# Kernel tuning notes

Hardware: AMD Instinct MI355X
Metric: run time of the kernel (lower is better)

## Reference

```python
import jax, jax.numpy as jnp
import numpy as np

ALPHA = 1.0

def setup_inputs() -> dict:
    key = jax.random.key(0)
    k1, k2 = jax.random.split(key)
    x = jax.random.normal(k1, (65536, 256), dtype=jnp.float32)
    clusters = jax.random.normal(k2, (512, 256), dtype=jnp.float32)
    return {"x": x, "clusters": clusters}

def reference(x, clusters):
    # squared L2 distance without materializing [B, K, D] broadcasts:
    # d[b,k] = |x_b|^2 + |c_k|^2 - 2 x_b . c_k
    x_sq = jnp.sum(x * x, axis=1, keepdims=True)            # [B, 1]
    c_sq = jnp.sum(clusters * clusters, axis=1)[None, :]    # [1, K]
    cross = jnp.einsum('bd,kd->bk', x, clusters)            # [B, K]
    d = x_sq + c_sq - 2.0 * cross                           # [B, K]
    # Student-t kernel soft assignment
    q = (1.0 + d / ALPHA) ** (-(ALPHA + 1.0) / 2.0)
    q = q / jnp.sum(q, axis=1, keepdims=True)
    return q
```

## Files before the change

kernel.cpp:

```cpp
#include <hip/hip_runtime.h>
#include <hip/hip_bf16.h>

typedef __attribute__((ext_vector_type(8))) short bf16x8;
typedef __attribute__((ext_vector_type(4))) float f32x4;

#define K_DIM 256
#define N_DIM 512
#define BM 32
#define M_DIM 65536
#define TPB 8
#define GRID (M_DIM / BM / TPB)

__device__ __forceinline__ unsigned short f2bf(float f) {
    unsigned int u = __float_as_uint(f);
    unsigned int r = (u + 0x7fffu + ((u >> 16) & 1u)) >> 16;
    return (unsigned short)r;
}

__global__ __launch_bounds__(256) void prep_clusters(
        const float* __restrict__ clusters,
        unsigned short* __restrict__ cba,
        float* __restrict__ csq) {
    const int row = blockIdx.x;
    const int t = threadIdx.x;
    const float v = clusters[row * K_DIM + t];
    const int wc = row >> 6, n = (row >> 4) & 3, r = row & 15;
    const int ks = t >> 5, kh = (t >> 3) & 3, ko = t & 7;
    cba[(size_t)wc * 16384 + ks * 2048 + n * 512 + (kh * 16 + r) * 8 + ko] = f2bf(v);
    float s = v * v;
    #pragma unroll
    for (int m = 1; m < 64; m <<= 1) s += __shfl_xor(s, m);
    __shared__ float red[4];
    if ((t & 63) == 0) red[t >> 6] = s;
    __syncthreads();
    if (t == 0) csq[row] = red[0] + red[1] + red[2] + red[3];
}

__global__ __launch_bounds__(512, 2) void cluster_q(
        const float* __restrict__ x,
        const unsigned short* __restrict__ cba,
        const float* __restrict__ csq,
        float* __restrict__ out) {
    __shared__ __align__(16) unsigned short xa[BM * K_DIM];
    __shared__ float xsq[BM];
    __shared__ __align__(16) float csql[N_DIM];
    __shared__ float rsum[8][BM];

    const int t = threadIdx.x;
    const int lane = t & 63;
    const int wc = t >> 6;

    const unsigned short* gsrc = cba + (size_t)wc * 16384;
    bf16x8 breg[8][4];
    #pragma unroll
    for (int ks = 0; ks < 8; ++ks)
        #pragma unroll
        for (int n = 0; n < 4; ++n)
            breg[ks][n] = *reinterpret_cast<const bf16x8*>(
                              gsrc + ks * 2048 + n * 512 + lane * 8);

    csql[t] = csq[t];

    const size_t base = (size_t)blockIdx.x * (TPB * BM);

    float4 xr0, xr1, xr2, xr3;
    {
        const float4* xp = reinterpret_cast<const float4*>(x + (base + wc) * K_DIM);
        xr0 = xp[lane];
        xr1 = xp[512 + lane];
        xr2 = xp[1024 + lane];
        xr3 = xp[1536 + lane];
    }

    for (int it = 0; it < TPB; ++it) {
        const size_t rowbase = base + (size_t)it * BM;

        const float4 vv[4] = {xr0, xr1, xr2, xr3};
        #pragma unroll
        for (int p = 0; p < 4; ++p) {
            const int row = wc + p * 8;
            const float4 v = vv[p];
            float s = v.x * v.x + v.y * v.y + v.z * v.z + v.w * v.w;
            #pragma unroll
            for (int m = 1; m < 64; m <<= 1) s += __shfl_xor(s, m);
            if (lane == 0) xsq[row] = s;
            const ushort4 pk = make_ushort4(f2bf(v.x), f2bf(v.y), f2bf(v.z), f2bf(v.w));
            const int swz = (lane * 8) ^ ((row & 7) << 4);
            *reinterpret_cast<ushort4*>(reinterpret_cast<char*>(xa) + row * 512 + swz) = pk;
        }
        __syncthreads();

        if (it + 1 < TPB) {
            const float4* xp = reinterpret_cast<const float4*>(
                                   x + (rowbase + BM + wc) * K_DIM);
            xr0 = xp[lane];
            xr1 = xp[512 + lane];
            xr2 = xp[1024 + lane];
            xr3 = xp[1536 + lane];
        }
        __builtin_amdgcn_sched_barrier(0);

        f32x4 acc[2][4];
        #pragma unroll
        for (int m = 0; m < 2; ++m)
            #pragma unroll
            for (int n = 0; n < 4; ++n)
                acc[m][n] = (f32x4){0.f, 0.f, 0.f, 0.f};

        #pragma unroll
        for (int ks = 0; ks < 8; ++ks) {
            const int r0 = (lane & 15);
            const int r1 = 16 + (lane & 15);
            const int c0 = (ks * 64 + (lane >> 4) * 16) ^ ((r0 & 7) << 4);
            const int c1 = (ks * 64 + (lane >> 4) * 16) ^ ((r1 & 7) << 4);
            const bf16x8 xm0 = *reinterpret_cast<const bf16x8*>(
                                   reinterpret_cast<const char*>(xa) + r0 * 512 + c0);
            const bf16x8 xm1 = *reinterpret_cast<const bf16x8*>(
                                   reinterpret_cast<const char*>(xa) + r1 * 512 + c1);
            #pragma unroll
            for (int n = 0; n < 4; ++n) {
                acc[0][n] = __builtin_amdgcn_mfma_f32_16x16x32_bf16(breg[ks][n], xm0, acc[0][n], 0, 0, 0);
                acc[1][n] = __builtin_amdgcn_mfma_f32_16x16x32_bf16(breg[ks][n], xm1, acc[1][n], 0, 0, 0);
            }
        }

        const float4* csql4 = reinterpret_cast<const float4*>(csql);
        float part[2] = {0.f, 0.f};
        #pragma unroll
        for (int m = 0; m < 2; ++m) {
            const float xs1 = 1.f + xsq[m * 16 + (lane & 15)];
            #pragma unroll
            for (int n = 0; n < 4; ++n) {
                const float4 cs = csql4[wc * 16 + n * 4 + (lane >> 4)];
                f32x4 q;
                q[0] = __builtin_amdgcn_rcpf(fmaf(-2.f, acc[m][n][0], xs1 + cs.x));
                q[1] = __builtin_amdgcn_rcpf(fmaf(-2.f, acc[m][n][1], xs1 + cs.y));
                q[2] = __builtin_amdgcn_rcpf(fmaf(-2.f, acc[m][n][2], xs1 + cs.z));
                q[3] = __builtin_amdgcn_rcpf(fmaf(-2.f, acc[m][n][3], xs1 + cs.w));
                acc[m][n] = q;
                part[m] += (q[0] + q[1]) + (q[2] + q[3]);
            }
        }
        #pragma unroll
        for (int m = 0; m < 2; ++m) {
            float s = part[m];
            s += __shfl_xor(s, 16);
            s += __shfl_xor(s, 32);
            if (lane < 16) rsum[wc][m * 16 + lane] = s;
        }
        __syncthreads();

        #pragma unroll
        for (int m = 0; m < 2; ++m) {
            const int b = m * 16 + (lane & 15);
            const float inv = __builtin_amdgcn_rcpf(
                ((rsum[0][b] + rsum[1][b]) + (rsum[2][b] + rsum[3][b])) +
                ((rsum[4][b] + rsum[5][b]) + (rsum[6][b] + rsum[7][b])));
            float* orow = out + (rowbase + b) * N_DIM + wc * 64 + (lane >> 4) * 4;
            #pragma unroll
            for (int n = 0; n < 4; ++n) {
                const f32x4 v = acc[m][n];
                float4 st = make_float4(v[0] * inv, v[1] * inv, v[2] * inv, v[3] * inv);
                *reinterpret_cast<float4*>(orow + n * 16) = st;
            }
        }
    }
}

extern "C" void kernel_launch(void* const* d_in, const int* in_sizes, int n_in,
                              void* d_out, int out_size, void* d_ws, size_t ws_size,
                              hipStream_t stream) {
    const float* x        = (const float*)d_in[0];
    const float* clusters = (const float*)d_in[1];
    float* out = (float*)d_out;
    unsigned short* cba = (unsigned short*)d_ws;
    float* csq = (float*)((char*)d_ws + (size_t)N_DIM * K_DIM * 2);
    prep_clusters<<<N_DIM, K_DIM, 0, stream>>>(clusters, cba, csq);
    cluster_q<<<GRID, 512, 0, stream>>>(x, cba, csq, out);
}
```

Measured before the change: 53.38 us.

## Double-buffer x tile in LDS and drop one barrier per iteration

The LDS tile of x (plus its row norms and the row-sum scratch) becomes double-buffered. The next tile is converted to bf16 and stored into the alternate buffer while the current one feeds the MFMAs, and global prefetch now runs two tiles ahead. This removes the per-iteration barrier that separated the x staging from the matmul, leaving one lightweight LDS-only barrier per iteration. It doubles the x-tile LDS footprint and keeps more registers live, which could affect occupancy at two blocks per CU.

```diff
diff --git a/kernel.cpp b/kernel.cpp
--- a/kernel.cpp
+++ b/kernel.cpp
@@ -15,6 +15,11 @@
     unsigned int u = __float_as_uint(f);
     unsigned int r = (u + 0x7fffu + ((u >> 16) & 1u)) >> 16;
     return (unsigned short)r;
+}
+
+__device__ __forceinline__ void barrier_lds() {
+    asm volatile("s_waitcnt lgkmcnt(0)" ::: "memory");
+    __builtin_amdgcn_s_barrier();
 }
 
 __global__ __launch_bounds__(256) void prep_clusters(
@@ -41,10 +46,10 @@
         const unsigned short* __restrict__ cba,
         const float* __restrict__ csq,
         float* __restrict__ out) {
-    __shared__ __align__(16) unsigned short xa[BM * K_DIM];
-    __shared__ float xsq[BM];
+    __shared__ __align__(16) unsigned short xa[2][BM * K_DIM];
+    __shared__ float xsq[2][BM];
     __shared__ __align__(16) float csql[N_DIM];
-    __shared__ float rsum[8][BM];
+    __shared__ float rsum[2][8][BM];
 
     const int t = threadIdx.x;
     const int lane = t & 63;
@@ -66,15 +71,9 @@
     float4 xr0, xr1, xr2, xr3;
     {
         const float4* xp = reinterpret_cast<const float4*>(x + (base + wc) * K_DIM);
-        xr0 = xp[lane];
-        xr1 = xp[512 + lane];
-        xr2 = xp[1024 + lane];
-        xr3 = xp[1536 + lane];
-    }
-
-    for (int it = 0; it < TPB; ++it) {
-        const size_t rowbase = base + (size_t)it * BM;
-
+        xr0 = xp[lane]; xr1 = xp[512 + lane]; xr2 = xp[1024 + lane]; xr3 = xp[1536 + lane];
+    }
+    {
         const float4 vv[4] = {xr0, xr1, xr2, xr3};
         #pragma unroll
         for (int p = 0; p < 4; ++p) {
@@ -83,20 +82,43 @@
             float s = v.x * v.x + v.y * v.y + v.z * v.z + v.w * v.w;
             #pragma unroll
             for (int m = 1; m < 64; m <<= 1) s += __shfl_xor(s, m);
-            if (lane == 0) xsq[row] = s;
+            if (lane == 0) xsq[0][row] = s;
             const ushort4 pk = make_ushort4(f2bf(v.x), f2bf(v.y), f2bf(v.z), f2bf(v.w));
             const int swz = (lane * 8) ^ ((row & 7) << 4);
-            *reinterpret_cast<ushort4*>(reinterpret_cast<char*>(xa) + row * 512 + swz) = pk;
-        }
-        __syncthreads();
+            *reinterpret_cast<ushort4*>(
+                reinterpret_cast<char*>(xa[0]) + row * 512 + swz) = pk;
+        }
+    }
+    {
+        const float4* xp = reinterpret_cast<const float4*>(x + (base + BM + wc) * K_DIM);
+        xr0 = xp[lane]; xr1 = xp[512 + lane]; xr2 = xp[1024 + lane]; xr3 = xp[1536 + lane];
+    }
+    barrier_lds();
+
+    for (int it = 0; it < TPB; ++it) {
+        const int cur = it & 1, nxt = cur ^ 1;
+        const size_t rowbase = base + (size_t)it * BM;
 
         if (it + 1 < TPB) {
+            const float4 vv[4] = {xr0, xr1, xr2, xr3};
+            #pragma unroll
+            for (int p = 0; p < 4; ++p) {
+                const int row = wc + p * 8;
+                const float4 v = vv[p];
+                float s = v.x * v.x + v.y * v.y + v.z * v.z + v.w * v.w;
+                #pragma unroll
+                for (int m = 1; m < 64; m <<= 1) s += __shfl_xor(s, m);
+                if (lane == 0) xsq[nxt][row] = s;
+                const ushort4 pk = make_ushort4(f2bf(v.x), f2bf(v.y), f2bf(v.z), f2bf(v.w));
+                const int swz = (lane * 8) ^ ((row & 7) << 4);
+                *reinterpret_cast<ushort4*>(
+                    reinterpret_cast<char*>(xa[nxt]) + row * 512 + swz) = pk;
+            }
+        }
+        if (it + 2 < TPB) {
             const float4* xp = reinterpret_cast<const float4*>(
-                                   x + (rowbase + BM + wc) * K_DIM);
-            xr0 = xp[lane];
-            xr1 = xp[512 + lane];
-            xr2 = xp[1024 + lane];
-            xr3 = xp[1536 + lane];
+                                   x + (rowbase + 2 * BM + wc) * K_DIM);
+            xr0 = xp[lane]; xr1 = xp[512 + lane]; xr2 = xp[1024 + lane]; xr3 = xp[1536 + lane];
         }
         __builtin_amdgcn_sched_barrier(0);
 
@@ -107,16 +129,15 @@
             for (int n = 0; n < 4; ++n)
                 acc[m][n] = (f32x4){0.f, 0.f, 0.f, 0.f};
 
+        const char* xab = reinterpret_cast<const char*>(xa[cur]);
         #pragma unroll
         for (int ks = 0; ks < 8; ++ks) {
             const int r0 = (lane & 15);
             const int r1 = 16 + (lane & 15);
             const int c0 = (ks * 64 + (lane >> 4) * 16) ^ ((r0 & 7) << 4);
             const int c1 = (ks * 64 + (lane >> 4) * 16) ^ ((r1 & 7) << 4);
-            const bf16x8 xm0 = *reinterpret_cast<const bf16x8*>(
-                                   reinterpret_cast<const char*>(xa) + r0 * 512 + c0);
-            const bf16x8 xm1 = *reinterpret_cast<const bf16x8*>(
-                                   reinterpret_cast<const char*>(xa) + r1 * 512 + c1);
+            const bf16x8 xm0 = *reinterpret_cast<const bf16x8*>(xab + r0 * 512 + c0);
+            const bf16x8 xm1 = *reinterpret_cast<const bf16x8*>(xab + r1 * 512 + c1);
             #pragma unroll
             for (int n = 0; n < 4; ++n) {
                 acc[0][n] = __builtin_amdgcn_mfma_f32_16x16x32_bf16(breg[ks][n], xm0, acc[0][n], 0, 0, 0);
@@ -128,7 +149,7 @@
         float part[2] = {0.f, 0.f};
         #pragma unroll
         for (int m = 0; m < 2; ++m) {
-            const float xs1 = 1.f + xsq[m * 16 + (lane & 15)];
+            const float xs1 = 1.f + xsq[cur][m * 16 + (lane & 15)];
             #pragma unroll
             for (int n = 0; n < 4; ++n) {
                 const float4 cs = csql4[wc * 16 + n * 4 + (lane >> 4)];
@@ -146,16 +167,16 @@
             float s = part[m];
             s += __shfl_xor(s, 16);
             s += __shfl_xor(s, 32);
-            if (lane < 16) rsum[wc][m * 16 + lane] = s;
-        }
-        __syncthreads();
+            if (lane < 16) rsum[cur][wc][m * 16 + lane] = s;
+        }
+        barrier_lds();
 
         #pragma unroll
         for (int m = 0; m < 2; ++m) {
             const int b = m * 16 + (lane & 15);
             const float inv = __builtin_amdgcn_rcpf(
-                ((rsum[0][b] + rsum[1][b]) + (rsum[2][b] + rsum[3][b])) +
-                ((rsum[4][b] + rsum[5][b]) + (rsum[6][b] + rsum[7][b])));
+                ((rsum[cur][0][b] + rsum[cur][1][b]) + (rsum[cur][2][b] + rsum[cur][3][b])) +
+                ((rsum[cur][4][b] + rsum[cur][5][b]) + (rsum[cur][6][b] + rsum[cur][7][b])));
             float* orow = out + (rowbase + b) * N_DIM + wc * 64 + (lane >> 4) * 4;
             #pragma unroll
             for (int n = 0; n < 4; ++n) {
```

Result: faster. 50.57 us (-5.3%).
